# Performance work log

Measured on AMD Instinct MI355X. Metric: run time of the kernel, lower is better.

Reference implementation:

```python
import jax, jax.numpy as jnp
import numpy as np

N, E, F_IN, EDIM, HEADS, DIM = 100000, 1600000, 128, 16, 4, 16
HC = HEADS * DIM


def add_self_loops_mean(src, dst, ea, n):
    # PyG add_self_loops with fill_value='mean': self-loop edge_attr is the mean
    # of incoming-edge attrs per target node (0 for isolated nodes).
    cnt = jax.ops.segment_sum(jnp.ones((dst.shape[0],), ea.dtype), dst, num_segments=n)
    sm = jax.ops.segment_sum(ea, dst, num_segments=n)
    loop = jnp.where(cnt[:, None] > 0, sm / jnp.maximum(cnt, 1.0)[:, None], 0.0)
    idx = jnp.arange(n, dtype=src.dtype)
    return (jnp.concatenate([src, idx]), jnp.concatenate([dst, idx]),
            jnp.concatenate([ea, loop], axis=0))


def gatv2(x, src, dst, ea, Wl, bl, Wr, br, We, att, bias):
    n = x.shape[0]
    h, c = att.shape
    xl = (x @ Wl + bl).reshape(n, h, c)   # source transform (lin_l)
    xr = (x @ Wr + br).reshape(n, h, c)   # target transform (lin_r)
    ee = (ea @ We).reshape(-1, h, c)      # edge transform (lin_edge, no bias)
    s = jax.nn.leaky_relu(xl[src] + xr[dst] + ee, negative_slope=0.2)  # [E,h,c]
    alpha = jnp.einsum('ehc,hc->eh', s, att)                           # [E,h]
    amax = jax.ops.segment_max(alpha, dst, num_segments=n)
    amax = jnp.where(jnp.isfinite(amax), amax, 0.0)
    ex = jnp.exp(alpha - amax[dst])
    denom = jax.ops.segment_sum(ex, dst, num_segments=n)
    a = ex / (denom[dst] + 1e-16)                                      # segment softmax
    out = jax.ops.segment_sum(xl[src] * a[:, :, None], dst, num_segments=n)
    return out.reshape(n, h * c) + bias


def setup_inputs() -> dict:
    key = jax.random.key(0)
    ks = jax.random.split(key, 24)
    s = 0.1
    d = {
        'x': jax.random.normal(ks[0], (N, F_IN), jnp.float32),
        'edge_index': jax.random.randint(ks[1], (2, E), 0, N, jnp.int32),
        'edge_attr': jax.random.normal(ks[2], (E, EDIM), jnp.float32),
        'Wl1': jax.random.normal(ks[3], (F_IN, HC)) * s, 'bl1': jnp.zeros((HC,)),
        'Wr1': jax.random.normal(ks[4], (F_IN, HC)) * s, 'br1': jnp.zeros((HC,)),
        'We1': jax.random.normal(ks[5], (EDIM, HC)) * s,
        'att1': jax.random.normal(ks[6], (HEADS, DIM)) * s,
        'bias1': jnp.zeros((HC,)),
        'Wl2': jax.random.normal(ks[7], (HC, HC)) * s, 'bl2': jnp.zeros((HC,)),
        'Wr2': jax.random.normal(ks[8], (HC, HC)) * s, 'br2': jnp.zeros((HC,)),
        'We2': jax.random.normal(ks[9], (EDIM, HC)) * s,
        'att2': jax.random.normal(ks[10], (HEADS, DIM)) * s,
        'bias2': jnp.zeros((HC,)),
        'W_lin1': jax.random.normal(ks[11], (HC, DIM)) * s, 'b_lin1': jnp.zeros((DIM,)),
        'W_lin2': jax.random.normal(ks[12], (DIM, 1)) * s, 'b_lin2': jnp.zeros((1,)),
    }
    return d


def reference(x, edge_index, edge_attr, Wl1, bl1, Wr1, br1, We1, att1, bias1,
              Wl2, bl2, Wr2, br2, We2, att2, bias2,
              W_lin1, b_lin1, W_lin2, b_lin2):
    src, dst, ea = add_self_loops_mean(edge_index[0], edge_index[1], edge_attr, x.shape[0])
    h = jax.nn.relu(gatv2(x, src, dst, ea, Wl1, bl1, Wr1, br1, We1, att1, bias1))
    h = jax.nn.relu(gatv2(h, src, dst, ea, Wl2, bl2, Wr2, br2, We2, att2, bias2))
    h = jax.nn.relu(h @ W_lin1 + b_lin1)
    # dropout p=0.1 is identity in eval mode
    out = jax.nn.sigmoid((h @ W_lin2 + b_lin2)[:, 0])
    return out
```

## Files before the change

kernel.cpp:

```cpp
#include <hip/hip_runtime.h>
#include <stdint.h>

typedef unsigned short u16;
typedef unsigned int u32;
typedef unsigned long long u64;

typedef __attribute__((ext_vector_type(8))) short bfrag;
typedef __attribute__((ext_vector_type(4))) float f32x4;

__device__ __forceinline__ float bf2f(u16 u) { return __uint_as_float(((u32)u) << 16); }
__device__ __forceinline__ u16 f2bf(float f) {
    u32 i = __float_as_uint(f);
    u32 r = i + 0x7fffu + ((i >> 16) & 1u);
    return (u16)(r >> 16);
}
__device__ __forceinline__ u32 pack2(float a, float b) {
    return (u32)f2bf(a) | ((u32)f2bf(b) << 16);
}
__device__ __forceinline__ float lo16(u32 u) { return __uint_as_float(u << 16); }
__device__ __forceinline__ float hi16(u32 u) { return __uint_as_float(u & 0xffff0000u); }
#define RFL(x) __builtin_amdgcn_readfirstlane(x)

#define DPP_ROR_ADD(p, ctrl) \
    p += __int_as_float(__builtin_amdgcn_update_dpp(0, __float_as_int(p), ctrl, 0xF, 0xF, false))
__device__ __forceinline__ float red16(float p) {
    DPP_ROR_ADD(p, 0x128);
    DPP_ROR_ADD(p, 0x124);
    DPP_ROR_ADD(p, 0x122);
    DPP_ROR_ADD(p, 0x121);
    return p;
}

__global__ void rank_hist(const int* __restrict__ dst, int E,
                          int* __restrict__ deg, int* __restrict__ rank) {
    int e = blockIdx.x * blockDim.x + threadIdx.x;
    if (e < E) rank[e] = atomicAdd(&deg[dst[e]], 1);
}

#define SCAN_T 256
#define SCAN_E 8
#define SCAN_CHUNK 2048

__global__ void scan_partial(const int* __restrict__ deg, int n, int* __restrict__ partials) {
    __shared__ int sh[SCAN_T];
    int b = blockIdx.x, t = threadIdx.x;
    int base = b * SCAN_CHUNK + t * SCAN_E;
    int s = 0;
#pragma unroll
    for (int i = 0; i < SCAN_E; i++) { int idx = base + i; if (idx < n) s += deg[idx]; }
    sh[t] = s; __syncthreads();
    for (int off = SCAN_T / 2; off > 0; off >>= 1) {
        if (t < off) sh[t] += sh[t + off];
        __syncthreads();
    }
    if (t == 0) partials[b] = sh[0];
}

__global__ void scan_mid(int* __restrict__ partials, int nb) {
    if (threadIdx.x == 0 && blockIdx.x == 0) {
        int acc = 0;
        for (int i = 0; i < nb; i++) { int v = partials[i]; partials[i] = acc; acc += v; }
    }
}

__global__ void scan_final(const int* __restrict__ deg, int n, const int* __restrict__ partials,
                           int* __restrict__ offs, int E) {
    __shared__ int sh[SCAN_T];
    int b = blockIdx.x, t = threadIdx.x;
    int base = b * SCAN_CHUNK + t * SCAN_E;
    int loc[SCAN_E];
    int s = 0;
#pragma unroll
    for (int i = 0; i < SCAN_E; i++) {
        int idx = base + i;
        int v = (idx < n) ? deg[idx] : 0;
        loc[i] = s; s += v;
    }
    sh[t] = s; __syncthreads();
    for (int off = 1; off < SCAN_T; off <<= 1) {
        int v = 0;
        if (t >= off) v = sh[t - off];
        __syncthreads();
        if (t >= off) sh[t] += v;
        __syncthreads();
    }
    int tbase = partials[b] + sh[t] - s;
#pragma unroll
    for (int i = 0; i < SCAN_E; i++) { int idx = base + i; if (idx < n) offs[idx] = tbase + loc[i]; }
    if (b == gridDim.x - 1 && t == SCAN_T - 1) offs[n] = E;
}

__global__ void csr_fill_idx(const int* __restrict__ srcv, const int* __restrict__ dstv,
                             const int* __restrict__ rank,
                             const int* __restrict__ offs, int E,
                             int2* __restrict__ cse) {
    int e = blockIdx.x * blockDim.x + threadIdx.x;
    if (e >= E) return;
    int d = dstv[e];
    int p = offs[d] + rank[e];
    cse[p] = make_int2(srcv[e], e);
}

__global__ void conv_attr(const float4* __restrict__ ea, int E, uint4* __restrict__ eattr) {
    int e = blockIdx.x * blockDim.x + threadIdx.x;
    if (e >= E) return;
    const float4* s = ea + (u64)e * 4;
    float4 v0 = s[0], v1 = s[1], v2 = s[2], v3 = s[3];
    eattr[(u64)e * 2]     = make_uint4(pack2(v0.x, v0.y), pack2(v0.z, v0.w),
                                       pack2(v1.x, v1.y), pack2(v1.z, v1.w));
    eattr[(u64)e * 2 + 1] = make_uint4(pack2(v2.x, v2.y), pack2(v2.z, v2.w),
                                       pack2(v3.x, v3.y), pack2(v3.z, v3.w));
}

template <int K>
__global__ void pack_w(const float* __restrict__ Wl, const float* __restrict__ Wr,
                       u32* __restrict__ Wb) {
    constexpr int NKS = K / 32;
    int t = blockIdx.x * blockDim.x + threadIdx.x;
    if (t >= 8 * NKS * 64) return;
    int lane = t & 63;
    int ks = (t >> 6) % NKS;
    int ct = (t >> 6) / NKS;
    int n = lane & 15, quad = lane >> 4;
    int c = ct * 16 + n;
    const float* W = (c < 64) ? Wl : Wr;
    int cc = c & 63;
    u32* d = Wb + (u64)t * 4;
#pragma unroll
    for (int p = 0; p < 4; p++) {
        int k0 = ks * 32 + quad * 8 + 2 * p;
        d[p] = pack2(W[(u64)k0 * 64 + cc], W[(u64)(k0 + 1) * 64 + cc]);
    }
}

__global__ void pack_we(const float* __restrict__ We, u32* __restrict__ web) {
    int t = blockIdx.x * blockDim.x + threadIdx.x;
    if (t >= 256) return;
    int lane = t & 63, ct = t >> 6;
    int n = lane & 15, quad = lane >> 4;
    int c = ct * 16 + n;
    u32* d = web + (u64)t * 4;
#pragma unroll
    for (int p = 0; p < 4; p++) {
        int k0 = quad * 8 + 2 * p;
        d[p] = (k0 + 1 < 16) ? pack2(We[(u64)k0 * 64 + c], We[(u64)(k0 + 1) * 64 + c]) : 0u;
    }
}

template <int K, bool XF32>
__global__ __launch_bounds__(256) void gemm_mfma(const void* __restrict__ Xv,
                                                 const u32* __restrict__ Wb,
                                                 const float* __restrict__ bl,
                                                 const float* __restrict__ br,
                                                 int N, u16* __restrict__ xl, u16* __restrict__ xr) {
    constexpr int NKS = K / 32;
    int lane = threadIdx.x & 63;
    int gw = (blockIdx.x * 256 + threadIdx.x) >> 6;
    int row0 = gw * 16;
    if (row0 >= N) return;
    int m = lane & 15, quad = lane >> 4;

    f32x4 acc[8];
#pragma unroll
    for (int ct = 0; ct < 8; ct++) acc[ct] = (f32x4){0.f, 0.f, 0.f, 0.f};

#pragma unroll
    for (int ks = 0; ks < NKS; ks++) {
        bfrag a;
        if (XF32) {
            const float* xp = (const float*)Xv + (u64)(row0 + m) * K + ks * 32 + quad * 8;
            float4 v0 = *(const float4*)xp;
            float4 v1 = *(const float4*)(xp + 4);
            union { bfrag v; u32 d[4]; } au;
            au.d[0] = pack2(v0.x, v0.y); au.d[1] = pack2(v0.z, v0.w);
            au.d[2] = pack2(v1.x, v1.y); au.d[3] = pack2(v1.z, v1.w);
            a = au.v;
        } else {
            a = *(const bfrag*)((const u16*)Xv + (u64)(row0 + m) * K + ks * 32 + quad * 8);
        }
#pragma unroll
        for (int ct = 0; ct < 8; ct++) {
            bfrag b = *(const bfrag*)(Wb + (u64)((ct * NKS + ks) * 64 + lane) * 4);
            acc[ct] = __builtin_amdgcn_mfma_f32_16x16x32_bf16(a, b, acc[ct], 0, 0, 0);
        }
    }

    float bvl[4], bvr[4];
#pragma unroll
    for (int ct = 0; ct < 4; ct++) { bvl[ct] = bl[ct * 16 + m]; bvr[ct] = br[ct * 16 + m]; }
#pragma unroll
    for (int r = 0; r < 4; r++) {
        int row = row0 + quad * 4 + r;
        uint2 ql, qr;
        ql.x = pack2(acc[0][r] + bvl[0], acc[1][r] + bvl[1]);
        ql.y = pack2(acc[2][r] + bvl[2], acc[3][r] + bvl[3]);
        qr.x = pack2(acc[4][r] + bvr[0], acc[5][r] + bvr[1]);
        qr.y = pack2(acc[6][r] + bvr[2], acc[7][r] + bvr[3]);
        *(uint2*)(xl + (u64)row * 64 + m * 4) = ql;
        *(uint2*)(xr + (u64)row * 64 + m * 4) = qr;
    }
}

__global__ __launch_bounds__(256) void gat_layer(const u16* __restrict__ xl, const u16* __restrict__ xr,
                                                 const int* __restrict__ offs,
                                                 const int2* __restrict__ cse,
                                                 const u32* __restrict__ eattr,
                                                 const u32* __restrict__ web,
                                                 const float* __restrict__ att,
                                                 const float* __restrict__ bias,
                                                 int N, u16* __restrict__ out) {
    const float LOG2E = 1.44269504088896340736f;
    int l = threadIdx.x & 63;
    int m = l & 15, quad = l >> 4;
    int wid = RFL((int)((blockIdx.x * 256 + threadIdx.x) >> 6));
    int nw = gridDim.x * 4;

    bfrag wb[4];
#pragma unroll
    for (int ct = 0; ct < 4; ct++) wb[ct] = *(const bfrag*)(web + (u64)(ct * 64 + l) * 4);

    float att_l = att[l] * LOG2E;
    float att_f[4];
#pragma unroll
    for (int ct = 0; ct < 4; ct++) att_f[ct] = att[ct * 16 + m] * LOG2E;
    float bias_l = bias[l];

    for (int n = wid; n < N; n += nw) {
        int a = RFL(offs[n]);
        int b = RFL(offs[n + 1]);
        float xr_l = bf2f(xr[(u32)(n * 64 + m * 4 + quad)]);
        float xl_self = bf2f(xl[(u32)(n * 64 + m * 4 + quad)]);
        uint2 qxr = *(const uint2*)(xr + (u32)(n * 64 + m * 4));
        float xr_f[4] = {lo16(qxr.x), hi16(qxr.x), lo16(qxr.y), hi16(qxr.y)};

        float o_f[4] = {0.f, 0.f, 0.f, 0.f};
        float ls_f[4] = {0.f, 0.f, 0.f, 0.f};
        float ee_f[4] = {0.f, 0.f, 0.f, 0.f};

        for (int base = a; base < b; base += 64) {
            int cnt64 = b - base; if (cnt64 > 64) cnt64 = 64;
            int idx = base + l;
            int2 sev = cse[idx < b ? idx : b - 1];
            int sv = sev.x, ev = sev.y;

            for (int j = 0; j < cnt64; j += 16) {
                int cnt = cnt64 - j; if (cnt > 16) cnt = 16;
                int em = __shfl(ev, j + m);
                union { bfrag v; u32 d[4]; } au;
                au.d[0] = 0; au.d[1] = 0; au.d[2] = 0; au.d[3] = 0;
                if (quad < 2 && m < cnt)
                    au.v = *(const bfrag*)(eattr + (u64)em * 8 + quad * 4);
                int jq = j + quad * 4;
                int sr0 = __shfl(sv, jq);
                int sr1 = __shfl(sv, jq + 1);
                int sr2 = __shfl(sv, jq + 2);
                int sr3 = __shfl(sv, jq + 3);
                uint2 g0 = *(const uint2*)(xl + (u32)(sr0 * 64 + m * 4));
                uint2 g1 = *(const uint2*)(xl + (u32)(sr1 * 64 + m * 4));
                uint2 g2 = *(const uint2*)(xl + (u32)(sr2 * 64 + m * 4));
                uint2 g3 = *(const uint2*)(xl + (u32)(sr3 * 64 + m * 4));
                float xv[4][4];
                xv[0][0] = lo16(g0.x); xv[0][1] = hi16(g0.x); xv[0][2] = lo16(g0.y); xv[0][3] = hi16(g0.y);
                xv[1][0] = lo16(g1.x); xv[1][1] = hi16(g1.x); xv[1][2] = lo16(g1.y); xv[1][3] = hi16(g1.y);
                xv[2][0] = lo16(g2.x); xv[2][1] = hi16(g2.x); xv[2][2] = lo16(g2.y); xv[2][3] = hi16(g2.y);
                xv[3][0] = lo16(g3.x); xv[3][1] = hi16(g3.x); xv[3][2] = lo16(g3.y); xv[3][3] = hi16(g3.y);
                f32x4 ee[4];
#pragma unroll
                for (int ct = 0; ct < 4; ct++) {
                    f32x4 c = (f32x4){xr_f[ct], xr_f[ct], xr_f[ct], xr_f[ct]};
                    ee[ct] = __builtin_amdgcn_mfma_f32_16x16x32_bf16(au.v, wb[ct], c, 0, 0, 0);
                }
#pragma unroll
                for (int ct = 0; ct < 4; ct++)
                    ee_f[ct] += (ee[ct][0] + ee[ct][1]) + (ee[ct][2] + ee[ct][3]) - 4.f * xr_f[ct];
                float zz[4][4];
#pragma unroll
                for (int ct = 0; ct < 4; ct++) {
#pragma unroll
                    for (int r = 0; r < 4; r++) {
                        float z = ee[ct][r] + xv[r][ct];
                        z = fmaxf(z, 0.2f * z);
                        zz[ct][r] = z * att_f[ct];
                    }
                }
#define R16(ctrl) { \
    DPP_ROR_ADD(zz[0][0], ctrl); DPP_ROR_ADD(zz[0][1], ctrl); DPP_ROR_ADD(zz[0][2], ctrl); DPP_ROR_ADD(zz[0][3], ctrl); \
    DPP_ROR_ADD(zz[1][0], ctrl); DPP_ROR_ADD(zz[1][1], ctrl); DPP_ROR_ADD(zz[1][2], ctrl); DPP_ROR_ADD(zz[1][3], ctrl); \
    DPP_ROR_ADD(zz[2][0], ctrl); DPP_ROR_ADD(zz[2][1], ctrl); DPP_ROR_ADD(zz[2][2], ctrl); DPP_ROR_ADD(zz[2][3], ctrl); \
    DPP_ROR_ADD(zz[3][0], ctrl); DPP_ROR_ADD(zz[3][1], ctrl); DPP_ROR_ADD(zz[3][2], ctrl); DPP_ROR_ADD(zz[3][3], ctrl); }
                R16(0x128) R16(0x124) R16(0x122) R16(0x121)
#undef R16
                float w[4][4];
#pragma unroll
                for (int ct = 0; ct < 4; ct++) {
#pragma unroll
                    for (int r = 0; r < 4; r++)
                        asm("v_exp_f32 %0, %1" : "=v"(w[ct][r]) : "v"(zz[ct][r]));
                }
                if (cnt < 16) {
#pragma unroll
                    for (int r = 0; r < 4; r++) {
                        bool ok = (quad * 4 + r) < cnt;
#pragma unroll
                        for (int ct = 0; ct < 4; ct++) w[ct][r] = ok ? w[ct][r] : 0.f;
                    }
                }
#pragma unroll
                for (int ct = 0; ct < 4; ct++) {
#pragma unroll
                    for (int r = 0; r < 4; r++) {
                        ls_f[ct] += w[ct][r];
                        o_f[ct] = fmaf(w[ct][r], xv[r][ct], o_f[ct]);
                    }
                }
            }
        }

#pragma unroll
        for (int ct = 0; ct < 4; ct++) {
            o_f[ct] += __shfl_xor(o_f[ct], 16);  o_f[ct] += __shfl_xor(o_f[ct], 32);
            ls_f[ct] += __shfl_xor(ls_f[ct], 16); ls_f[ct] += __shfl_xor(ls_f[ct], 32);
            ee_f[ct] += __shfl_xor(ee_f[ct], 16); ee_f[ct] += __shfl_xor(ee_f[ct], 32);
        }
        float o    = (quad & 2) ? ((quad & 1) ? o_f[3] : o_f[2]) : ((quad & 1) ? o_f[1] : o_f[0]);
        float lsum = (quad & 2) ? ((quad & 1) ? ls_f[3] : ls_f[2]) : ((quad & 1) ? ls_f[1] : ls_f[0]);
        float eesum= (quad & 2) ? ((quad & 1) ? ee_f[3] : ee_f[2]) : ((quad & 1) ? ee_f[1] : ee_f[0]);

        int deg = b - a;
        float inv = (deg > 0) ? 1.f / (float)deg : 0.f;
        float z = (eesum * inv + xr_l) + xl_self;
        z = fmaxf(z, 0.2f * z);
        float vv = red16(z * att_l);
        float ws;
        asm("v_exp_f32 %0, %1" : "=v"(ws) : "v"(vv));
        lsum += ws;
        o = fmaf(ws, xl_self, o);

        float res = o / (lsum + 1e-16f) + bias_l;
        res = fmaxf(res, 0.f);
        out[(u32)(n * 64 + l)] = f2bf(res);
    }
}

__global__ __launch_bounds__(256) void mlp_head(const u16* __restrict__ h,
                                                const float* __restrict__ W1, const float* __restrict__ b1,
                                                const float* __restrict__ W2, const float* __restrict__ b2,
                                                int N, float* __restrict__ out) {
    __shared__ float w1[64 * 16];
    __shared__ float sb1[16];
    __shared__ float w2[16];
    for (int i = threadIdx.x; i < 64 * 16; i += 256) w1[i] = W1[i];
    if (threadIdx.x < 16) { sb1[threadIdx.x] = b1[threadIdx.x]; w2[threadIdx.x] = W2[threadIdx.x]; }
    __syncthreads();
    float b2v = b2[0];
    int n = blockIdx.x * blockDim.x + threadIdx.x;
    if (n < N) {
        float hv[64];
        const u32* hp = (const u32*)(h + (u64)n * 64);
#pragma unroll
        for (int i = 0; i < 32; i++) { u32 u = hp[i]; hv[2 * i] = lo16(u); hv[2 * i + 1] = hi16(u); }
        float z = b2v;
        for (int j = 0; j < 16; j++) {
            float acc = sb1[j];
#pragma unroll
            for (int k = 0; k < 64; k++) acc = fmaf(hv[k], w1[k * 16 + j], acc);
            acc = fmaxf(acc, 0.f);
            z = fmaf(acc, w2[j], z);
        }
        out[n] = 1.f / (1.f + __expf(-z));
    }
}

extern "C" void kernel_launch(void* const* d_in, const int* in_sizes, int n_in,
                              void* d_out, int out_size, void* d_ws, size_t ws_size,
                              hipStream_t stream) {
    const float* x    = (const float*)d_in[0];
    const int*   ei   = (const int*)d_in[1];
    const float* ea   = (const float*)d_in[2];
    const float* Wl1  = (const float*)d_in[3];
    const float* bl1  = (const float*)d_in[4];
    const float* Wr1  = (const float*)d_in[5];
    const float* br1  = (const float*)d_in[6];
    const float* We1  = (const float*)d_in[7];
    const float* att1 = (const float*)d_in[8];
    const float* bias1= (const float*)d_in[9];
    const float* Wl2  = (const float*)d_in[10];
    const float* bl2  = (const float*)d_in[11];
    const float* Wr2  = (const float*)d_in[12];
    const float* br2  = (const float*)d_in[13];
    const float* We2  = (const float*)d_in[14];
    const float* att2 = (const float*)d_in[15];
    const float* bias2= (const float*)d_in[16];
    const float* W1   = (const float*)d_in[17];
    const float* b1   = (const float*)d_in[18];
    const float* W2   = (const float*)d_in[19];
    const float* b2   = (const float*)d_in[20];
    float* out = (float*)d_out;

    const int N = in_sizes[0] / 128;
    const int E = in_sizes[1] / 2;
    const int* srcv = ei;
    const int* dstv = ei + E;

    uint8_t* p = (uint8_t*)d_ws;
    auto carve = [&](size_t bytes) -> void* {
        void* r = (void*)p;
        p += (bytes + 255) & ~(size_t)255;
        return r;
    };
    int*  deg     = (int*)carve((size_t)N * 4);
    int*  rank    = (int*)carve((size_t)E * 4);
    int*  offs    = (int*)carve((size_t)(N + 1) * 4);
    int*  partials= (int*)carve(4096);
    int2* cse     = (int2*)carve((size_t)E * 8);
    u32*  eattr   = (u32*)carve((size_t)E * 32);
    u16*  xl      = (u16*)carve((size_t)N * 64 * 2);
    u16*  xr      = (u16*)carve((size_t)N * 64 * 2);
    u16*  hb      = (u16*)carve((size_t)N * 64 * 2);
    u32*  wb1     = (u32*)carve(8 * 4 * 64 * 16);
    u32*  wb2     = (u32*)carve(8 * 2 * 64 * 16);
    u32*  web1    = (u32*)carve(4 * 64 * 4 * 4);
    u32*  web2    = (u32*)carve(4 * 64 * 4 * 4);
    (void)ws_size; (void)n_in; (void)out_size;

    hipMemsetAsync(deg, 0, (size_t)N * 4, stream);

    const int B = 256;
    pack_w<128><<<8, 256, 0, stream>>>(Wl1, Wr1, wb1);
    pack_w<64><<<4, 256, 0, stream>>>(Wl2, Wr2, wb2);
    pack_we<<<1, 256, 0, stream>>>(We1, web1);
    pack_we<<<1, 256, 0, stream>>>(We2, web2);
    conv_attr<<<(E + B - 1) / B, B, 0, stream>>>((const float4*)ea, E, (uint4*)eattr);

    rank_hist<<<(E + B - 1) / B, B, 0, stream>>>(dstv, E, deg, rank);
    int nb = (N + SCAN_CHUNK - 1) / SCAN_CHUNK;
    scan_partial<<<nb, SCAN_T, 0, stream>>>(deg, N, partials);
    scan_mid<<<1, 64, 0, stream>>>(partials, nb);
    scan_final<<<nb, SCAN_T, 0, stream>>>(deg, N, partials, offs, E);
    csr_fill_idx<<<(E + B - 1) / B, B, 0, stream>>>(srcv, dstv, rank, offs, E, cse);

    int gemm_blocks = (N / 16 + 3) / 4;
    gemm_mfma<128, true><<<gemm_blocks, 256, 0, stream>>>(x, wb1, bl1, br1, N, xl, xr);
    gat_layer<<<8192, 256, 0, stream>>>(xl, xr, offs, cse, eattr, web1,
                                        att1, bias1, N, hb);
    gemm_mfma<64, false><<<gemm_blocks, 256, 0, stream>>>(hb, wb2, bl2, br2, N, xl, xr);
    gat_layer<<<8192, 256, 0, stream>>>(xl, xr, offs, cse, eattr, web2,
                                        att2, bias2, N, hb);
    mlp_head<<<(N + B - 1) / B, B, 0, stream>>>(hb, W1, b1, W2, b2, N, out);
}
```

Measured before the change: 602.4 us.

## Fuse prep kernels, store edge ids only in CSR, pack GAT math into float2

The edge attribute conversion is merged into the degree/rank histogram kernel, and the four weight-packing kernels are merged into one launch, cutting launch count and one pass over the edge list. The CSR now stores only edge ids, so the src index is gathered from the original edge list inside the GAT layer, trading a smaller CSR write for an extra dependent gather. The GAT inner loop is rewritten with float2 vector types so the compiler can emit packed FP32 adds, multiplies and FMAs. The MFMA now accumulates from zero, and xr is added afterwards instead of being folded into the accumulator.

```diff
diff --git a/kernel.cpp b/kernel.cpp
--- a/kernel.cpp
+++ b/kernel.cpp
@@ -7,6 +7,7 @@
 
 typedef __attribute__((ext_vector_type(8))) short bfrag;
 typedef __attribute__((ext_vector_type(4))) float f32x4;
+typedef __attribute__((ext_vector_type(2))) float f32x2;
 
 __device__ __forceinline__ float bf2f(u16 u) { return __uint_as_float(((u32)u) << 16); }
 __device__ __forceinline__ u16 f2bf(float f) {
@@ -31,10 +32,20 @@
     return p;
 }
 
-__global__ void rank_hist(const int* __restrict__ dst, int E,
-                          int* __restrict__ deg, int* __restrict__ rank) {
+__global__ void edge_prep(const int* __restrict__ dstv, const float4* __restrict__ ea, int E,
+                          int* __restrict__ deg, int* __restrict__ rank,
+                          uint4* __restrict__ eattr) {
     int e = blockIdx.x * blockDim.x + threadIdx.x;
-    if (e < E) rank[e] = atomicAdd(&deg[dst[e]], 1);
+    if (e >= E) return;
+    const float4* s = ea + (u64)e * 4;
+    float4 v0 = s[0], v1 = s[1], v2 = s[2], v3 = s[3];
+    int d = dstv[e];
+    int r = atomicAdd(&deg[d], 1);
+    eattr[(u64)e * 2]     = make_uint4(pack2(v0.x, v0.y), pack2(v0.z, v0.w),
+                                       pack2(v1.x, v1.y), pack2(v1.z, v1.w));
+    eattr[(u64)e * 2 + 1] = make_uint4(pack2(v2.x, v2.y), pack2(v2.z, v2.w),
+                                       pack2(v3.x, v3.y), pack2(v3.z, v3.w));
+    rank[e] = r;
 }
 
 #define SCAN_T 256
@@ -90,34 +101,17 @@
     if (b == gridDim.x - 1 && t == SCAN_T - 1) offs[n] = E;
 }
 
-__global__ void csr_fill_idx(const int* __restrict__ srcv, const int* __restrict__ dstv,
+__global__ void csr_fill_idx(const int* __restrict__ dstv,
                              const int* __restrict__ rank,
                              const int* __restrict__ offs, int E,
-                             int2* __restrict__ cse) {
+                             int* __restrict__ ceid) {
     int e = blockIdx.x * blockDim.x + threadIdx.x;
     if (e >= E) return;
-    int d = dstv[e];
-    int p = offs[d] + rank[e];
-    cse[p] = make_int2(srcv[e], e);
-}
-
-__global__ void conv_attr(const float4* __restrict__ ea, int E, uint4* __restrict__ eattr) {
-    int e = blockIdx.x * blockDim.x + threadIdx.x;
-    if (e >= E) return;
-    const float4* s = ea + (u64)e * 4;
-    float4 v0 = s[0], v1 = s[1], v2 = s[2], v3 = s[3];
-    eattr[(u64)e * 2]     = make_uint4(pack2(v0.x, v0.y), pack2(v0.z, v0.w),
-                                       pack2(v1.x, v1.y), pack2(v1.z, v1.w));
-    eattr[(u64)e * 2 + 1] = make_uint4(pack2(v2.x, v2.y), pack2(v2.z, v2.w),
-                                       pack2(v3.x, v3.y), pack2(v3.z, v3.w));
-}
-
-template <int K>
-__global__ void pack_w(const float* __restrict__ Wl, const float* __restrict__ Wr,
-                       u32* __restrict__ Wb) {
-    constexpr int NKS = K / 32;
-    int t = blockIdx.x * blockDim.x + threadIdx.x;
-    if (t >= 8 * NKS * 64) return;
+    ceid[offs[dstv[e]] + rank[e]] = e;
+}
+
+__device__ __forceinline__ void pack_w_job(const float* Wl, const float* Wr, u32* Wb,
+                                           int t, int NKS) {
     int lane = t & 63;
     int ks = (t >> 6) % NKS;
     int ct = (t >> 6) / NKS;
@@ -132,10 +126,7 @@
         d[p] = pack2(W[(u64)k0 * 64 + cc], W[(u64)(k0 + 1) * 64 + cc]);
     }
 }
-
-__global__ void pack_we(const float* __restrict__ We, u32* __restrict__ web) {
-    int t = blockIdx.x * blockDim.x + threadIdx.x;
-    if (t >= 256) return;
+__device__ __forceinline__ void pack_we_job(const float* We, u32* web, int t) {
     int lane = t & 63, ct = t >> 6;
     int n = lane & 15, quad = lane >> 4;
     int c = ct * 16 + n;
@@ -145,6 +136,17 @@
         int k0 = quad * 8 + 2 * p;
         d[p] = (k0 + 1 < 16) ? pack2(We[(u64)k0 * 64 + c], We[(u64)(k0 + 1) * 64 + c]) : 0u;
     }
+}
+__global__ void pack_all(const float* __restrict__ Wl1, const float* __restrict__ Wr1,
+                         const float* __restrict__ Wl2, const float* __restrict__ Wr2,
+                         const float* __restrict__ We1, const float* __restrict__ We2,
+                         u32* __restrict__ wb1, u32* __restrict__ wb2,
+                         u32* __restrict__ web1, u32* __restrict__ web2) {
+    int t = blockIdx.x * blockDim.x + threadIdx.x;
+    if (t < 2048)       pack_w_job(Wl1, Wr1, wb1, t, 4);
+    else if (t < 3072)  pack_w_job(Wl2, Wr2, wb2, t - 2048, 2);
+    else if (t < 3328)  pack_we_job(We1, web1, t - 3072);
+    else if (t < 3584)  pack_we_job(We2, web2, t - 3328);
 }
 
 template <int K, bool XF32>
@@ -203,7 +205,8 @@
 
 __global__ __launch_bounds__(256) void gat_layer(const u16* __restrict__ xl, const u16* __restrict__ xr,
                                                  const int* __restrict__ offs,
-                                                 const int2* __restrict__ cse,
+                                                 const int* __restrict__ ceid,
+                                                 const int* __restrict__ srcv,
                                                  const u32* __restrict__ eattr,
                                                  const u32* __restrict__ web,
                                                  const float* __restrict__ att,
@@ -221,8 +224,12 @@
 
     float att_l = att[l] * LOG2E;
     float att_f[4];
-#pragma unroll
-    for (int ct = 0; ct < 4; ct++) att_f[ct] = att[ct * 16 + m] * LOG2E;
+    f32x2 att2[4];
+#pragma unroll
+    for (int ct = 0; ct < 4; ct++) {
+        att_f[ct] = att[ct * 16 + m] * LOG2E;
+        att2[ct] = (f32x2){att_f[ct], att_f[ct]};
+    }
     float bias_l = bias[l];
 
     for (int n = wid; n < N; n += nw) {
@@ -231,17 +238,23 @@
         float xr_l = bf2f(xr[(u32)(n * 64 + m * 4 + quad)]);
         float xl_self = bf2f(xl[(u32)(n * 64 + m * 4 + quad)]);
         uint2 qxr = *(const uint2*)(xr + (u32)(n * 64 + m * 4));
-        float xr_f[4] = {lo16(qxr.x), hi16(qxr.x), lo16(qxr.y), hi16(qxr.y)};
-
-        float o_f[4] = {0.f, 0.f, 0.f, 0.f};
-        float ls_f[4] = {0.f, 0.f, 0.f, 0.f};
-        float ee_f[4] = {0.f, 0.f, 0.f, 0.f};
+        f32x2 xr2[4];
+        xr2[0] = (f32x2){lo16(qxr.x), lo16(qxr.x)};
+        xr2[1] = (f32x2){hi16(qxr.x), hi16(qxr.x)};
+        xr2[2] = (f32x2){lo16(qxr.y), lo16(qxr.y)};
+        xr2[3] = (f32x2){hi16(qxr.y), hi16(qxr.y)};
+
+        f32x2 o2[4], ls2[4], ee2[4];
+#pragma unroll
+        for (int ct = 0; ct < 4; ct++) {
+            o2[ct] = (f32x2){0.f, 0.f}; ls2[ct] = (f32x2){0.f, 0.f}; ee2[ct] = (f32x2){0.f, 0.f};
+        }
 
         for (int base = a; base < b; base += 64) {
             int cnt64 = b - base; if (cnt64 > 64) cnt64 = 64;
             int idx = base + l;
-            int2 sev = cse[idx < b ? idx : b - 1];
-            int sv = sev.x, ev = sev.y;
+            int ev = ceid[idx < b ? idx : b - 1];
+            int sv = srcv[ev];
 
             for (int j = 0; j < cnt64; j += 16) {
                 int cnt = cnt64 - j; if (cnt > 16) cnt = 16;
@@ -259,29 +272,29 @@
                 uint2 g1 = *(const uint2*)(xl + (u32)(sr1 * 64 + m * 4));
                 uint2 g2 = *(const uint2*)(xl + (u32)(sr2 * 64 + m * 4));
                 uint2 g3 = *(const uint2*)(xl + (u32)(sr3 * 64 + m * 4));
-                float xv[4][4];
-                xv[0][0] = lo16(g0.x); xv[0][1] = hi16(g0.x); xv[0][2] = lo16(g0.y); xv[0][3] = hi16(g0.y);
-                xv[1][0] = lo16(g1.x); xv[1][1] = hi16(g1.x); xv[1][2] = lo16(g1.y); xv[1][3] = hi16(g1.y);
-                xv[2][0] = lo16(g2.x); xv[2][1] = hi16(g2.x); xv[2][2] = lo16(g2.y); xv[2][3] = hi16(g2.y);
-                xv[3][0] = lo16(g3.x); xv[3][1] = hi16(g3.x); xv[3][2] = lo16(g3.y); xv[3][3] = hi16(g3.y);
+                f32x2 xv01[4], xv23[4];
+                xv01[0] = (f32x2){lo16(g0.x), lo16(g1.x)}; xv23[0] = (f32x2){lo16(g2.x), lo16(g3.x)};
+                xv01[1] = (f32x2){hi16(g0.x), hi16(g1.x)}; xv23[1] = (f32x2){hi16(g2.x), hi16(g3.x)};
+                xv01[2] = (f32x2){lo16(g0.y), lo16(g1.y)}; xv23[2] = (f32x2){lo16(g2.y), lo16(g3.y)};
+                xv01[3] = (f32x2){hi16(g0.y), hi16(g1.y)}; xv23[3] = (f32x2){hi16(g2.y), hi16(g3.y)};
+                const f32x4 zero4 = (f32x4){0.f, 0.f, 0.f, 0.f};
                 f32x4 ee[4];
 #pragma unroll
+                for (int ct = 0; ct < 4; ct++)
+                    ee[ct] = __builtin_amdgcn_mfma_f32_16x16x32_bf16(au.v, wb[ct], zero4, 0, 0, 0);
+                float zz[4][4];
+#pragma unroll
                 for (int ct = 0; ct < 4; ct++) {
-                    f32x4 c = (f32x4){xr_f[ct], xr_f[ct], xr_f[ct], xr_f[ct]};
-                    ee[ct] = __builtin_amdgcn_mfma_f32_16x16x32_bf16(au.v, wb[ct], c, 0, 0, 0);
-                }
-#pragma unroll
-                for (int ct = 0; ct < 4; ct++)
-                    ee_f[ct] += (ee[ct][0] + ee[ct][1]) + (ee[ct][2] + ee[ct][3]) - 4.f * xr_f[ct];
-                float zz[4][4];
-#pragma unroll
-                for (int ct = 0; ct < 4; ct++) {
-#pragma unroll
-                    for (int r = 0; r < 4; r++) {
-                        float z = ee[ct][r] + xv[r][ct];
-                        z = fmaxf(z, 0.2f * z);
-                        zz[ct][r] = z * att_f[ct];
-                    }
+                    f32x2 e01 = (f32x2){ee[ct][0], ee[ct][1]};
+                    f32x2 e23 = (f32x2){ee[ct][2], ee[ct][3]};
+                    ee2[ct] += e01 + e23;
+                    f32x2 z01 = (e01 + xr2[ct]) + xv01[ct];
+                    f32x2 z23 = (e23 + xr2[ct]) + xv23[ct];
+                    f32x2 m01 = z01 * 0.2f;
+                    f32x2 m23 = z23 * 0.2f;
+                    f32x2 l01 = (f32x2){fmaxf(z01.x, m01.x), fmaxf(z01.y, m01.y)} * att2[ct];
+                    f32x2 l23 = (f32x2){fmaxf(z23.x, m23.x), fmaxf(z23.y, m23.y)} * att2[ct];
+                    zz[ct][0] = l01.x; zz[ct][1] = l01.y; zz[ct][2] = l23.x; zz[ct][3] = l23.y;
                 }
 #define R16(ctrl) { \
     DPP_ROR_ADD(zz[0][0], ctrl); DPP_ROR_ADD(zz[0][1], ctrl); DPP_ROR_ADD(zz[0][2], ctrl); DPP_ROR_ADD(zz[0][3], ctrl); \
@@ -307,15 +320,22 @@
                 }
 #pragma unroll
                 for (int ct = 0; ct < 4; ct++) {
-#pragma unroll
-                    for (int r = 0; r < 4; r++) {
-                        ls_f[ct] += w[ct][r];
-                        o_f[ct] = fmaf(w[ct][r], xv[r][ct], o_f[ct]);
-                    }
+                    f32x2 w01 = (f32x2){w[ct][0], w[ct][1]};
+                    f32x2 w23 = (f32x2){w[ct][2], w[ct][3]};
+                    ls2[ct] += w01 + w23;
+                    o2[ct] = __builtin_elementwise_fma(w01, xv01[ct], o2[ct]);
+                    o2[ct] = __builtin_elementwise_fma(w23, xv23[ct], o2[ct]);
                 }
             }
         }
 
+        float o_f[4], ls_f[4], ee_f[4];
+#pragma unroll
+        for (int ct = 0; ct < 4; ct++) {
+            o_f[ct] = o2[ct].x + o2[ct].y;
+            ls_f[ct] = ls2[ct].x + ls2[ct].y;
+            ee_f[ct] = ee2[ct].x + ee2[ct].y;
+        }
 #pragma unroll
         for (int ct = 0; ct < 4; ct++) {
             o_f[ct] += __shfl_xor(o_f[ct], 16);  o_f[ct] += __shfl_xor(o_f[ct], 32);
@@ -412,7 +432,7 @@
     int*  rank    = (int*)carve((size_t)E * 4);
     int*  offs    = (int*)carve((size_t)(N + 1) * 4);
     int*  partials= (int*)carve(4096);
-    int2* cse     = (int2*)carve((size_t)E * 8);
+    int*  ceid    = (int*)carve((size_t)E * 4);
     u32*  eattr   = (u32*)carve((size_t)E * 32);
     u16*  xl      = (u16*)carve((size_t)N * 64 * 2);
     u16*  xr      = (u16*)carve((size_t)N * 64 * 2);
@@ -426,25 +446,20 @@
     hipMemsetAsync(deg, 0, (size_t)N * 4, stream);
 
     const int B = 256;
-    pack_w<128><<<8, 256, 0, stream>>>(Wl1, Wr1, wb1);
-    pack_w<64><<<4, 256, 0, stream>>>(Wl2, Wr2, wb2);
-    pack_we<<<1, 256, 0, stream>>>(We1, web1);
-    pack_we<<<1, 256, 0, stream>>>(We2, web2);
-    conv_attr<<<(E + B - 1) / B, B, 0, stream>>>((const float4*)ea, E, (uint4*)eattr);
-
-    rank_hist<<<(E + B - 1) / B, B, 0, stream>>>(dstv, E, deg, rank);
+    pack_all<<<14, 256, 0, stream>>>(Wl1, Wr1, Wl2, Wr2, We1, We2, wb1, wb2, web1, web2);
+    edge_prep<<<(E + B - 1) / B, B, 0, stream>>>(dstv, (const float4*)ea, E, deg, rank, (uint4*)eattr);
     int nb = (N + SCAN_CHUNK - 1) / SCAN_CHUNK;
     scan_partial<<<nb, SCAN_T, 0, stream>>>(deg, N, partials);
     scan_mid<<<1, 64, 0, stream>>>(partials, nb);
     scan_final<<<nb, SCAN_T, 0, stream>>>(deg, N, partials, offs, E);
-    csr_fill_idx<<<(E + B - 1) / B, B, 0, stream>>>(srcv, dstv, rank, offs, E, cse);
+    csr_fill_idx<<<(E + B - 1) / B, B, 0, stream>>>(dstv, rank, offs, E, ceid);
 
     int gemm_blocks = (N / 16 + 3) / 4;
     gemm_mfma<128, true><<<gemm_blocks, 256, 0, stream>>>(x, wb1, bl1, br1, N, xl, xr);
-    gat_layer<<<8192, 256, 0, stream>>>(xl, xr, offs, cse, eattr, web1,
+    gat_layer<<<8192, 256, 0, stream>>>(xl, xr, offs, ceid, srcv, eattr, web1,
                                         att1, bias1, N, hb);
     gemm_mfma<64, false><<<gemm_blocks, 256, 0, stream>>>(hb, wb2, bl2, br2, N, xl, xr);
-    gat_layer<<<8192, 256, 0, stream>>>(xl, xr, offs, cse, eattr, web2,
+    gat_layer<<<8192, 256, 0, stream>>>(xl, xr, offs, ceid, srcv, eattr, web2,
                                         att2, bias2, N, hb);
     mlp_head<<<(N + B - 1) / B, B, 0, stream>>>(hb, W1, b1, W2, b2, N, out);
 }
```

After: 598.2 us. No clear change (-0.7%).
